# Optimization experiments

Hardware: AMD Instinct MI355X
Metric: run time of the kernel (lower is better)

Reference implementation:

```python
import jax, jax.numpy as jnp
import numpy as np

T, B, E = 2048, 2, 1024
H = 16
D = E // H


def setup_inputs() -> dict:
    key = jax.random.key(0)
    ks = jax.random.split(key, 7)
    s = 1.0 / np.sqrt(E)
    return {
        "query": jax.random.normal(ks[0], (T, B, E), jnp.float32),
        "key": jax.random.normal(ks[1], (T, B, E), jnp.float32),
        "value": jax.random.normal(ks[2], (T, B, E), jnp.float32),
        "in_proj_weight": jax.random.normal(ks[3], (3 * E, E), jnp.float32) * s,
        "in_proj_bias": jax.random.normal(ks[4], (3 * E,), jnp.float32) * 0.02,
        "out_proj_weight": jax.random.normal(ks[5], (E, E), jnp.float32) * s,
        "out_proj_bias": jax.random.normal(ks[6], (E,), jnp.float32) * 0.02,
    }


def reference(query, key, value, in_proj_weight, in_proj_bias, out_proj_weight, out_proj_bias):
    tgt_len, bsz, embed_dim = query.shape
    src_len = key.shape[0]
    head_dim = embed_dim // H
    # packed in-projection (F.linear: x @ W.T + b)
    w_q, w_k, w_v = jnp.split(in_proj_weight, 3, axis=0)
    b_q, b_k, b_v = jnp.split(in_proj_bias, 3, axis=0)
    q = query @ w_q.T + b_q   # [T, B, E]
    k = key @ w_k.T + b_k     # [S, B, E]
    v = value @ w_v.T + b_v   # [S, B, E]
    # [T,B,E] -> [B,H,T,D]
    q = q.reshape(tgt_len, bsz, H, head_dim).transpose(1, 2, 0, 3)
    k = k.reshape(src_len, bsz, H, head_dim).transpose(1, 2, 0, 3)
    v = v.reshape(src_len, bsz, H, head_dim).transpose(1, 2, 0, 3)
    scale = 1.0 / jnp.sqrt(jnp.asarray(head_dim, q.dtype))
    scores = jnp.einsum("bhtd,bhsd->bhts", q, k) * scale  # [B,H,T,S]
    attn_weights = jax.nn.softmax(scores, axis=-1)
    attn = jnp.einsum("bhts,bhsd->bhtd", attn_weights, v)  # [B,H,T,D]
    # [B,H,T,D] -> [T,B,E]
    attn = attn.transpose(2, 0, 1, 3).reshape(tgt_len, bsz, embed_dim)
    attn_output = attn @ out_proj_weight.T + out_proj_bias  # [T,B,E]
    # averaged attention weights over heads (average_attn_weights=True)
    avg_weights = jnp.sum(attn_weights, axis=1) / H  # [B,T,S]
    return attn_output, avg_weights
```

## Files before the change

### kernel.cpp

```cpp
#include <hip/hip_runtime.h>
#include <hip/hip_bf16.h>

typedef float  f32x2  __attribute__((ext_vector_type(2)));
typedef float  f32x4  __attribute__((ext_vector_type(4)));
typedef float  f32x16 __attribute__((ext_vector_type(16)));
typedef __bf16 bf16x8 __attribute__((ext_vector_type(8)));

#define MFMA16(A,B,C) __builtin_amdgcn_mfma_f32_16x16x32_bf16((A),(B),(C),0,0,0)
#define MFMA32(A,B,C) __builtin_amdgcn_mfma_f32_32x32x16_bf16((A),(B),(C),0,0,0)
#define EXP2(x) __builtin_amdgcn_exp2f(x)
#define LOG2(x) __builtin_amdgcn_logf(x)

static constexpr int Tn = 2048, Bn = 2, En = 1024, Hn = 16, Dn = 64;
static constexpr float kQScale = 0.125f * 1.4426950408889634f;

static __device__ __forceinline__ unsigned pack2(float a, float b) {
  union { __bf16 h[2]; unsigned u; } un;
  un.h[0] = (__bf16)a; un.h[1] = (__bf16)b;
  return un.u;
}

static __device__ __forceinline__ void gload_lds16(const void* g, void* l) {
  __builtin_amdgcn_global_load_lds(
      (const __attribute__((address_space(1))) void*)g,
      (__attribute__((address_space(3))) void*)l, 16, 0, 0);
}

__global__ __launch_bounds__(256)
void k_cvt(const float* __restrict__ q, const float* __restrict__ k,
           const float* __restrict__ v, const float* __restrict__ w3,
           const float* __restrict__ wo,
           __bf16* __restrict__ qb, __bf16* __restrict__ kb,
           __bf16* __restrict__ vb, __bf16* __restrict__ w3b,
           __bf16* __restrict__ wob)
{
  const size_t g = (size_t)blockIdx.x * 256 + threadIdx.x;
  const float* src;
  __bf16* dst;
  size_t off;
  if (g < 524288)        { src = q;  dst = qb;  off = g; }
  else if (g < 1048576)  { src = k;  dst = kb;  off = g - 524288; }
  else if (g < 1572864)  { src = v;  dst = vb;  off = g - 1048576; }
  else if (g < 1966080)  { src = w3; dst = w3b; off = g - 1572864; }
  else                   { src = wo; dst = wob; off = g - 1966080; }
  const float* p = src + off * 8;
  f32x4 a = *reinterpret_cast<const f32x4*>(p);
  f32x4 b = *reinterpret_cast<const f32x4*>(p + 4);
  bf16x8 o;
  #pragma unroll
  for (int e = 0; e < 4; ++e) { o[e] = (__bf16)a[e]; o[e + 4] = (__bf16)b[e]; }
  *reinterpret_cast<bf16x8*>(dst + off * 8) = o;
}

__global__ __launch_bounds__(256)
void k_qkv(const __bf16* __restrict__ Xq, const __bf16* __restrict__ Xk,
           const __bf16* __restrict__ Xv, const __bf16* __restrict__ W,
           const float* __restrict__ bias,
           __bf16* __restrict__ q_ws, __bf16* __restrict__ k_ws,
           __bf16* __restrict__ v_ws)
{
  __shared__ __align__(16) char a_lds[8192];
  __shared__ __align__(16) char b_lds[8192];
  const int tid = threadIdx.x;
  const int lane = tid & 63, w = tid >> 6;
  const int wr = w >> 1, wc = w & 1;
  const int ag = lane >> 4, lr = lane & 15;
  const int mBase = blockIdx.x * 128;
  const int oBase = blockIdx.y * 128;
  const int which = blockIdx.y >> 3;
  const __bf16* X  = (which == 0) ? Xq : ((which == 1) ? Xk : Xv);
  const __bf16* Wt = W + (size_t)oBase * En;
  __bf16* dst = (which == 0) ? q_ws : ((which == 1) ? k_ws : v_ws);
  const float oscale = (which == 0) ? kQScale : 1.0f;

  const int gA = w;
  char* laA0 = a_lds + gA * 2048;
  char* laA1 = a_lds + gA * 2048 + 1024;
  char* lbA0 = b_lds + gA * 2048;
  char* lbA1 = b_lds + gA * 2048 + 1024;
  const __bf16* pa0 = X  + (size_t)(mBase + lane) * En + gA * 8;
  const __bf16* pa1 = X  + (size_t)(mBase + 64 + lane) * En + gA * 8;
  const __bf16* pb0 = Wt + (size_t)(lane) * En + gA * 8;
  const __bf16* pb1 = Wt + (size_t)(64 + lane) * En + gA * 8;

  f32x4 acc[4][4];
  #pragma unroll
  for (int i = 0; i < 4; ++i)
    #pragma unroll
    for (int j = 0; j < 4; ++j) { f32x4 z = {0.f, 0.f, 0.f, 0.f}; acc[i][j] = z; }

  for (int kk = 0; kk < En; kk += 32) {
    __syncthreads();
    gload_lds16(pa0 + kk, laA0);
    gload_lds16(pa1 + kk, laA1);
    gload_lds16(pb0 + kk, lbA0);
    gload_lds16(pb1 + kk, lbA1);
    __syncthreads();
    bf16x8 af[4], bfr[4];
    #pragma unroll
    for (int mb = 0; mb < 4; ++mb)
      af[mb] = *(const bf16x8*)(a_lds + ag * 2048 + (wr * 64 + mb * 16 + lr) * 16);
    #pragma unroll
    for (int nb = 0; nb < 4; ++nb)
      bfr[nb] = *(const bf16x8*)(b_lds + ag * 2048 + (wc * 64 + nb * 16 + lr) * 16);
    #pragma unroll
    for (int mb = 0; mb < 4; ++mb)
      #pragma unroll
      for (int nb = 0; nb < 4; ++nb)
        acc[mb][nb] = MFMA16(af[mb], bfr[nb], acc[mb][nb]);
  }

  #pragma unroll
  for (int nb = 0; nb < 4; ++nb) {
    int oG = oBase + wc * 64 + nb * 16 + lr;
    float bv = bias[oG];
    int oS = oG & (En - 1);
    int h = oS >> 6, d = oS & 63;
    #pragma unroll
    for (int mb = 0; mb < 4; ++mb)
      #pragma unroll
      for (int r = 0; r < 4; ++r) {
        int i = mBase + wr * 64 + mb * 16 + ag * 4 + r;
        int t = i >> 1, b2 = i & 1;
        dst[(((size_t)(b2 * Hn + h)) * Tn + t) * Dn + d] =
            (__bf16)((acc[mb][nb][r] + bv) * oscale);
      }
  }
}

__global__ __launch_bounds__(256)
void k_transpose_v(const __bf16* __restrict__ v_ws, __bf16* __restrict__ vt_ws)
{
  __shared__ __bf16 tile[64][72];
  const int bh = blockIdx.x >> 5;
  const int tt = blockIdx.x & 31;
  const int tid = threadIdx.x;
  const __bf16* src = v_ws + ((size_t)bh * Tn + tt * 64) * Dn;
  #pragma unroll
  for (int it = 0; it < 2; ++it) {
    int gi = tid + it * 256;
    int row = gi >> 3, gg = gi & 7;
    *reinterpret_cast<bf16x8*>(&tile[row][gg * 8]) =
        *reinterpret_cast<const bf16x8*>(src + row * Dn + gg * 8);
  }
  __syncthreads();
  __bf16* dst = vt_ws + (size_t)bh * Dn * Tn + tt * 64;
  #pragma unroll
  for (int it = 0; it < 2; ++it) {
    int gi = tid + it * 256;
    int drow = gi >> 3, tg = gi & 7;
    bf16x8 vv;
    #pragma unroll
    for (int e = 0; e < 8; ++e) vv[e] = tile[tg * 8 + e][drow];
    *reinterpret_cast<bf16x8*>(dst + (size_t)drow * Tn + tg * 8) = vv;
  }
}

__global__ __launch_bounds__(256, 2)
void k_flash(const __bf16* __restrict__ q_ws, const __bf16* __restrict__ k_ws,
             const __bf16* __restrict__ vt_ws, __bf16* __restrict__ ctx,
             float* __restrict__ stats)
{
  __shared__ __align__(16) char kv_sm[2 * 16384];

  const int tid = threadIdx.x;
  const int lane = tid & 63, w = tid >> 6;
  const int tl = lane & 31, hi = lane >> 5;
  const int bh = blockIdx.x >> 4;
  const int qt = blockIdx.x & 15;
  const int t0w = qt * 128 + w * 32;

  const __bf16* kbase  = k_ws + (size_t)bh * Tn * Dn;
  const __bf16* vtbase = vt_ws + (size_t)bh * Dn * Tn;

  bf16x8 qf[4];
  {
    const __bf16* qrow = q_ws + ((size_t)bh * Tn + t0w + tl) * Dn + hi * 8;
    #pragma unroll
    for (int c = 0; c < 4; ++c)
      qf[c] = *reinterpret_cast<const bf16x8*>(qrow + c * 16);
  }

  f32x16 accO0, accO1;
  #pragma unroll
  for (int i = 0; i < 16; ++i) { accO0[i] = 0.f; accO1[i] = 0.f; }
  float m_run = -INFINITY, l_run = 0.f;

  const int r0 = tid >> 3, s0 = tid & 7;
  const int ldso = ((s0 ^ (r0 & 7)) << 4);
  const int ko0 = r0 * 128 + ldso;

  bf16x8 rk0 = *(const bf16x8*)(kbase + r0 * 64 + s0 * 8);
  bf16x8 rk1 = *(const bf16x8*)(kbase + (r0 + 32) * 64 + s0 * 8);
  bf16x8 rv0 = *(const bf16x8*)(vtbase + (size_t)r0 * Tn + s0 * 8);
  bf16x8 rv1 = *(const bf16x8*)(vtbase + (size_t)(r0 + 32) * Tn + s0 * 8);
  *(bf16x8*)(kv_sm + ko0) = rk0;
  *(bf16x8*)(kv_sm + ko0 + 4096) = rk1;
  *(bf16x8*)(kv_sm + 8192 + ko0) = rv0;
  *(bf16x8*)(kv_sm + 8192 + ko0 + 4096) = rv1;

  for (int st = 0; st < 32; ++st) {
    __syncthreads();
    const char* cur = kv_sm + (st & 1) * 16384;
    char* nxt = kv_sm + ((st + 1) & 1) * 16384;
    if (st + 1 < 32) {
      const __bf16* kn = kbase + (size_t)(st + 1) * 64 * Dn;
      const __bf16* vn = vtbase + (st + 1) * 64;
      rk0 = *(const bf16x8*)(kn + r0 * 64 + s0 * 8);
      rk1 = *(const bf16x8*)(kn + (r0 + 32) * 64 + s0 * 8);
      rv0 = *(const bf16x8*)(vn + (size_t)r0 * Tn + s0 * 8);
      rv1 = *(const bf16x8*)(vn + (size_t)(r0 + 32) * Tn + s0 * 8);
    }

    f32x16 sc0, sc1;
    #pragma unroll
    for (int i = 0; i < 16; ++i) { sc0[i] = 0.f; sc1[i] = 0.f; }
    const char* kr0 = cur + tl * 128;
    const char* kr1 = cur + (32 + tl) * 128;
    __builtin_amdgcn_s_setprio(1);
    #pragma unroll
    for (int c = 0; c < 4; ++c) {
      const int off = (((2 * c + hi) ^ (tl & 7)) << 4);
      sc0 = MFMA32(*(const bf16x8*)(kr0 + off), qf[c], sc0);
      sc1 = MFMA32(*(const bf16x8*)(kr1 + off), qf[c], sc1);
    }
    __builtin_amdgcn_s_setprio(0);

    float mx[8];
    #pragma unroll
    for (int i = 0; i < 8; ++i)
      mx[i] = fmaxf(fmaxf(sc0[i], sc0[i + 8]), fmaxf(sc1[i], sc1[i + 8]));
    float tm = fmaxf(fmaxf(fmaxf(mx[0], mx[1]), fmaxf(mx[2], mx[3])),
                     fmaxf(fmaxf(mx[4], mx[5]), fmaxf(mx[6], mx[7])));
    tm = fmaxf(tm, __shfl_xor(tm, 32, 64));
    if (__any(tm > m_run + 8.0f)) {
      const float mn = fmaxf(m_run, tm);
      const float es = EXP2(m_run - mn);
      m_run = mn;
      l_run *= es;
      #pragma unroll
      for (int q = 0; q < 4; ++q)
        #pragma unroll
        for (int rr = 0; rr < 4; ++rr) {
          const float e = __shfl(es, 8 * q + 4 * hi + rr, 32);
          accO0[q * 4 + rr] *= e;
          accO1[q * 4 + rr] *= e;
        }
    }
    #pragma unroll
    for (int i = 0; i < 16; ++i) {
      sc0[i] = EXP2(sc0[i] - m_run);
      sc1[i] = EXP2(sc1[i] - m_run);
    }
    float p0s = 0.f, p1s = 0.f, p2s = 0.f, p3s = 0.f;
    #pragma unroll
    for (int i = 0; i < 16; i += 4) {
      p0s += sc0[i]     + sc1[i];
      p1s += sc0[i + 1] + sc1[i + 1];
      p2s += sc0[i + 2] + sc1[i + 2];
      p3s += sc0[i + 3] + sc1[i + 3];
    }
    float rs = (p0s + p1s) + (p2s + p3s);
    rs += __shfl_xor(rs, 32, 64);
    l_run += rs;

    unsigned wA0[4], wB0[4], wA1[4], wB1[4];
    #pragma unroll
    for (int g = 0; g < 4; ++g) {
      wA0[g] = pack2(sc0[4 * g],     sc0[4 * g + 1]);
      wB0[g] = pack2(sc0[4 * g + 2], sc0[4 * g + 3]);
      wA1[g] = pack2(sc1[4 * g],     sc1[4 * g + 1]);
      wB1[g] = pack2(sc1[4 * g + 2], sc1[4 * g + 3]);
    }
    bf16x8 pa[2][2];
    #pragma unroll
    for (int sb = 0; sb < 2; ++sb) {
      const unsigned* WA = sb ? wA1 : wA0;
      const unsigned* WB = sb ? wB1 : wB0;
      #pragma unroll
      for (int c = 0; c < 2; ++c) {
        unsigned a0 = WA[2 * c], a1 = WA[2 * c + 1];
        unsigned b0 = WB[2 * c], b1 = WB[2 * c + 1];
        unsigned xa0 = __shfl_xor(a0, 32, 64);
        unsigned xa1 = __shfl_xor(a1, 32, 64);
        unsigned xb0 = __shfl_xor(b0, 32, 64);
        unsigned xb1 = __shfl_xor(b1, 32, 64);
        union { unsigned u[4]; bf16x8 v; } uu;
        uu.u[0] = hi ? xa1 : a0;
        uu.u[1] = hi ? xb1 : b0;
        uu.u[2] = hi ? a1 : xa0;
        uu.u[3] = hi ? b1 : xb0;
        pa[sb][c] = uu.v;
      }
    }

    const char* vr0 = cur + 8192 + tl * 128;
    const char* vr1 = cur + 8192 + (32 + tl) * 128;
    __builtin_amdgcn_s_setprio(1);
    #pragma unroll
    for (int sb = 0; sb < 2; ++sb)
      #pragma unroll
      for (int c = 0; c < 2; ++c) {
        const int off = (((sb * 4 + c * 2 + hi) ^ (tl & 7)) << 4);
        accO0 = MFMA32(pa[sb][c], *(const bf16x8*)(vr0 + off), accO0);
        accO1 = MFMA32(pa[sb][c], *(const bf16x8*)(vr1 + off), accO1);
      }
    __builtin_amdgcn_s_setprio(0);

    if (st + 1 < 32) {
      *(bf16x8*)(nxt + ko0) = rk0;
      *(bf16x8*)(nxt + ko0 + 4096) = rk1;
      *(bf16x8*)(nxt + 8192 + ko0) = rv0;
      *(bf16x8*)(nxt + 8192 + ko0 + 4096) = rv1;
    }
  }

  const float linv = 1.0f / l_run;
  const int b2 = bh >> 4, h = bh & 15;
  #pragma unroll
  for (int q = 0; q < 4; ++q)
    #pragma unroll
    for (int rr = 0; rr < 4; ++rr) {
      const float lv = __shfl(linv, 8 * q + 4 * hi + rr, 32);
      const int t = t0w + 8 * q + 4 * hi + rr;
      __bf16* cp = ctx + ((size_t)t * Bn + b2) * En + h * 64 + tl;
      cp[0]  = (__bf16)(accO0[q * 4 + rr] * lv);
      cp[32] = (__bf16)(accO1[q * 4 + rr] * lv);
    }
  if (hi == 0) {
    const int t = t0w + tl;
    f32x2 stv; stv[0] = m_run; stv[1] = l_run;
    *reinterpret_cast<f32x2*>(&stats[((size_t)bh * Tn + t) * 2]) = stv;
  }
}

__global__ __launch_bounds__(256)
void k_avgw(const __bf16* __restrict__ q_ws, const __bf16* __restrict__ k_ws,
            const float* __restrict__ stats, float* __restrict__ avg_out)
{
  __shared__ __align__(16) char q_sm[8192];
  __shared__ __align__(16) char k_sm[8192];
  __shared__ __align__(16) float adj_sm[16][64];

  const int tid = threadIdx.x;
  const int lane = tid & 63, w = tid >> 6;
  const int tl = lane & 31, hi = lane >> 5;
  const int b2 = blockIdx.x >> 10;
  const int tt = (blockIdx.x >> 5) & 31;
  const int ss = blockIdx.x & 31;
  const int thalf = (w >> 1) * 32, shalf = (w & 1) * 32;

  #pragma unroll
  for (int it = 0; it < 4; ++it) {
    int idx = tid + it * 256;
    int h = idx >> 6, trow = idx & 63;
    f32x2 sv = *(const f32x2*)&stats[(((size_t)(b2 * Hn + h)) * Tn + tt * 64 + trow) * 2];
    adj_sm[h][trow] = sv[0] + LOG2(16.0f * sv[1]);
  }

  const size_t hstride = (size_t)Tn * Dn;
  const __bf16* qb = q_ws + ((size_t)(b2 * Hn) * Tn + tt * 64) * Dn;
  const __bf16* kb = k_ws + ((size_t)(b2 * Hn) * Tn + ss * 64) * Dn;

  const int r0 = tid >> 3, s0 = tid & 7;
  const int ldso = ((s0 ^ (r0 & 7)) << 4);
  const int ko0 = r0 * 128 + ldso, ko1 = ko0 + 32 * 128;

  bf16x8 rq0 = *(const bf16x8*)(qb + r0 * 64 + s0 * 8);
  bf16x8 rq1 = *(const bf16x8*)(qb + (r0 + 32) * 64 + s0 * 8);
  bf16x8 rk0 = *(const bf16x8*)(kb + r0 * 64 + s0 * 8);
  bf16x8 rk1 = *(const bf16x8*)(kb + (r0 + 32) * 64 + s0 * 8);

  f32x16 avg;
  #pragma unroll
  for (int i = 0; i < 16; ++i) avg[i] = 0.f;

  const char* qr = q_sm + (thalf + tl) * 128;
  const char* kr = k_sm + (shalf + tl) * 128;

  for (int h = 0; h < Hn; ++h) {
    __syncthreads();
    *(bf16x8*)(q_sm + ko0) = rq0;
    *(bf16x8*)(q_sm + ko1) = rq1;
    *(bf16x8*)(k_sm + ko0) = rk0;
    *(bf16x8*)(k_sm + ko1) = rk1;
    __syncthreads();
    if (h + 1 < Hn) {
      const __bf16* qn = qb + (size_t)(h + 1) * hstride;
      const __bf16* kn = kb + (size_t)(h + 1) * hstride;
      rq0 = *(const bf16x8*)(qn + r0 * 64 + s0 * 8);
      rq1 = *(const bf16x8*)(qn + (r0 + 32) * 64 + s0 * 8);
      rk0 = *(const bf16x8*)(kn + r0 * 64 + s0 * 8);
      rk1 = *(const bf16x8*)(kn + (r0 + 32) * 64 + s0 * 8);
    }

    f32x16 sc;
    #pragma unroll
    for (int i = 0; i < 16; ++i) sc[i] = 0.f;
    #pragma unroll
    for (int c = 0; c < 4; ++c) {
      const int off = (((2 * c + hi) ^ (tl & 7)) << 4);
      sc = MFMA32(*(const bf16x8*)(qr + off), *(const bf16x8*)(kr + off), sc);
    }

    #pragma unroll
    for (int q = 0; q < 4; ++q) {
      f32x4 ad = *(const f32x4*)&adj_sm[h][thalf + 8 * q + 4 * hi];
      #pragma unroll
      for (int r = 0; r < 4; ++r)
        avg[q * 4 + r] += EXP2(sc[q * 4 + r] - ad[r]);
    }
  }

  #pragma unroll
  for (int q = 0; q < 4; ++q)
    #pragma unroll
    for (int r = 0; r < 4; ++r) {
      int t = tt * 64 + thalf + 8 * q + 4 * hi + r;
      int s = ss * 64 + shalf + tl;
      avg_out[((size_t)(b2 * Tn + t)) * Tn + s] = avg[q * 4 + r];
    }
}

__global__ __launch_bounds__(256)
void k_outproj(const __bf16* __restrict__ ctx, const __bf16* __restrict__ W,
               const float* __restrict__ bias, float* __restrict__ out)
{
  __shared__ __align__(16) char a_lds[8192];
  __shared__ __align__(16) char b_lds[8192];
  const int tid = threadIdx.x;
  const int lane = tid & 63, w = tid >> 6;
  const int wr = w >> 1, wc = w & 1;
  const int ag = lane >> 4, lr = lane & 15;
  const int mBase = blockIdx.x * 128;
  const int oBase = blockIdx.y * 128;
  const __bf16* Wt = W + (size_t)oBase * En;

  const int gA = w;
  char* laA0 = a_lds + gA * 2048;
  char* laA1 = a_lds + gA * 2048 + 1024;
  char* lbA0 = b_lds + gA * 2048;
  char* lbA1 = b_lds + gA * 2048 + 1024;
  const __bf16* pa0 = ctx + (size_t)(mBase + lane) * En + gA * 8;
  const __bf16* pa1 = ctx + (size_t)(mBase + 64 + lane) * En + gA * 8;
  const __bf16* pb0 = Wt + (size_t)(lane) * En + gA * 8;
  const __bf16* pb1 = Wt + (size_t)(64 + lane) * En + gA * 8;

  f32x4 acc[4][4];
  #pragma unroll
  for (int i = 0; i < 4; ++i)
    #pragma unroll
    for (int j = 0; j < 4; ++j) { f32x4 z = {0.f,0.f,0.f,0.f}; acc[i][j] = z; }

  for (int kk = 0; kk < En; kk += 32) {
    __syncthreads();
    gload_lds16(pa0 + kk, laA0);
    gload_lds16(pa1 + kk, laA1);
    gload_lds16(pb0 + kk, lbA0);
    gload_lds16(pb1 + kk, lbA1);
    __syncthreads();
    bf16x8 af[4], bfr[4];
    #pragma unroll
    for (int mb = 0; mb < 4; ++mb)
      af[mb] = *(const bf16x8*)(a_lds + ag * 2048 + (wr * 64 + mb * 16 + lr) * 16);
    #pragma unroll
    for (int nb = 0; nb < 4; ++nb)
      bfr[nb] = *(const bf16x8*)(b_lds + ag * 2048 + (wc * 64 + nb * 16 + lr) * 16);
    #pragma unroll
    for (int mb = 0; mb < 4; ++mb)
      #pragma unroll
      for (int nb = 0; nb < 4; ++nb)
        acc[mb][nb] = MFMA16(af[mb], bfr[nb], acc[mb][nb]);
  }

  #pragma unroll
  for (int nb = 0; nb < 4; ++nb) {
    int o = oBase + wc * 64 + nb * 16 + lr;
    float bv = bias[o];
    #pragma unroll
    for (int mb = 0; mb < 4; ++mb)
      #pragma unroll
      for (int r = 0; r < 4; ++r) {
        int i = mBase + wr * 64 + mb * 16 + ag * 4 + r;
        out[(size_t)i * En + o] = acc[mb][nb][r] + bv;
      }
  }
}

extern "C" void kernel_launch(void* const* d_in, const int* in_sizes, int n_in,
                              void* d_out, int out_size, void* d_ws, size_t ws_size,
                              hipStream_t stream)
{
  (void)in_sizes; (void)n_in; (void)out_size; (void)ws_size;
  const float* query = (const float*)d_in[0];
  const float* key   = (const float*)d_in[1];
  const float* value = (const float*)d_in[2];
  const float* in_w  = (const float*)d_in[3];
  const float* in_b  = (const float*)d_in[4];
  const float* out_w = (const float*)d_in[5];
  const float* out_b = (const float*)d_in[6];

  float* attn_out = (float*)d_out;
  float* avg_out  = (float*)d_out + (size_t)Tn * Bn * En;

  char* ws = (char*)d_ws;
  const size_t MB = 1u << 20;
  __bf16* q_ws  = (__bf16*)(ws);
  __bf16* k_ws  = (__bf16*)(ws + 8 * MB);
  __bf16* v_ws  = (__bf16*)(ws + 16 * MB);
  __bf16* vt_ws = (__bf16*)(ws + 24 * MB);
  __bf16* ctx   = (__bf16*)(ws + 32 * MB);
  float*  stats = (float*)(ws + 40 * MB);
  __bf16* xq_bf = vt_ws;
  __bf16* xk_bf = ctx;
  __bf16* xv_bf = (__bf16*)(ws + 40 * MB + 512 * 1024);
  __bf16* w3_bf = (__bf16*)(ws + 48 * MB + 512 * 1024);
  __bf16* wo_bf = (__bf16*)(ws + 54 * MB + 512 * 1024);

  k_cvt<<<8192, 256, 0, stream>>>(query, key, value, in_w, out_w,
                                  xq_bf, xk_bf, xv_bf, w3_bf, wo_bf);
  k_qkv<<<dim3(32, 24), 256, 0, stream>>>(xq_bf, xk_bf, xv_bf, w3_bf, in_b,
                                          q_ws, k_ws, v_ws);
  k_transpose_v<<<1024, 256, 0, stream>>>(v_ws, vt_ws);
  k_flash<<<512, 256, 0, stream>>>(q_ws, k_ws, vt_ws, ctx, stats);
  k_avgw<<<2048, 256, 0, stream>>>(q_ws, k_ws, stats, avg_out);
  k_outproj<<<dim3(32, 8), 256, 0, stream>>>(ctx, wo_bf, out_b, attn_out);
}
```

Before: 212.5 us.

## Double-buffer GEMM/avgw LDS, compute softmax rowsum via MFMA, use permlane32 swap

The QKV and output-projection GEMMs get double-buffered LDS with prefetch of the next K tile, which removes one barrier per step. The attention-weight kernel likewise double-buffers its Q/K tiles across heads. In the flash kernel the row sum is now accumulated by an extra MFMA against a ones vector instead of a VALU reduction plus shuffle. The P-fragment repack uses v_permlane32_swap instead of four cross-lane shuffles, and the flash kernel precomputes the per-row log-sum adjustment so avgw reads one float. This adds LDS usage and extra MFMA work per iteration in exchange for fewer VALU ops and barriers.

```diff
diff --git a/kernel.cpp b/kernel.cpp
--- a/kernel.cpp
+++ b/kernel.cpp
@@ -59,8 +59,8 @@
            __bf16* __restrict__ q_ws, __bf16* __restrict__ k_ws,
            __bf16* __restrict__ v_ws)
 {
-  __shared__ __align__(16) char a_lds[8192];
-  __shared__ __align__(16) char b_lds[8192];
+  __shared__ __align__(16) char a_lds[2][8192];
+  __shared__ __align__(16) char b_lds[2][8192];
   const int tid = threadIdx.x;
   const int lane = tid & 63, w = tid >> 6;
   const int wr = w >> 1, wc = w & 1;
@@ -74,10 +74,6 @@
   const float oscale = (which == 0) ? kQScale : 1.0f;
 
   const int gA = w;
-  char* laA0 = a_lds + gA * 2048;
-  char* laA1 = a_lds + gA * 2048 + 1024;
-  char* lbA0 = b_lds + gA * 2048;
-  char* lbA1 = b_lds + gA * 2048 + 1024;
   const __bf16* pa0 = X  + (size_t)(mBase + lane) * En + gA * 8;
   const __bf16* pa1 = X  + (size_t)(mBase + 64 + lane) * En + gA * 8;
   const __bf16* pb0 = Wt + (size_t)(lane) * En + gA * 8;
@@ -89,25 +85,34 @@
     #pragma unroll
     for (int j = 0; j < 4; ++j) { f32x4 z = {0.f, 0.f, 0.f, 0.f}; acc[i][j] = z; }
 
-  for (int kk = 0; kk < En; kk += 32) {
-    __syncthreads();
-    gload_lds16(pa0 + kk, laA0);
-    gload_lds16(pa1 + kk, laA1);
-    gload_lds16(pb0 + kk, lbA0);
-    gload_lds16(pb1 + kk, lbA1);
-    __syncthreads();
+  gload_lds16(pa0, &a_lds[0][gA * 2048]);
+  gload_lds16(pa1, &a_lds[0][gA * 2048 + 1024]);
+  gload_lds16(pb0, &b_lds[0][gA * 2048]);
+  gload_lds16(pb1, &b_lds[0][gA * 2048 + 1024]);
+  __syncthreads();
+
+  for (int kt = 0; kt < 32; ++kt) {
+    const int cur = kt & 1, nxt = cur ^ 1;
+    if (kt + 1 < 32) {
+      const int kk = (kt + 1) * 32;
+      gload_lds16(pa0 + kk, &a_lds[nxt][gA * 2048]);
+      gload_lds16(pa1 + kk, &a_lds[nxt][gA * 2048 + 1024]);
+      gload_lds16(pb0 + kk, &b_lds[nxt][gA * 2048]);
+      gload_lds16(pb1 + kk, &b_lds[nxt][gA * 2048 + 1024]);
+    }
     bf16x8 af[4], bfr[4];
     #pragma unroll
     for (int mb = 0; mb < 4; ++mb)
-      af[mb] = *(const bf16x8*)(a_lds + ag * 2048 + (wr * 64 + mb * 16 + lr) * 16);
+      af[mb] = *(const bf16x8*)(&a_lds[cur][ag * 2048 + (wr * 64 + mb * 16 + lr) * 16]);
     #pragma unroll
     for (int nb = 0; nb < 4; ++nb)
-      bfr[nb] = *(const bf16x8*)(b_lds + ag * 2048 + (wc * 64 + nb * 16 + lr) * 16);
+      bfr[nb] = *(const bf16x8*)(&b_lds[cur][ag * 2048 + (wc * 64 + nb * 16 + lr) * 16]);
     #pragma unroll
     for (int mb = 0; mb < 4; ++mb)
       #pragma unroll
       for (int nb = 0; nb < 4; ++nb)
         acc[mb][nb] = MFMA16(af[mb], bfr[nb], acc[mb][nb]);
+    __syncthreads();
   }
 
   #pragma unroll
@@ -159,7 +164,7 @@
 __global__ __launch_bounds__(256, 2)
 void k_flash(const __bf16* __restrict__ q_ws, const __bf16* __restrict__ k_ws,
              const __bf16* __restrict__ vt_ws, __bf16* __restrict__ ctx,
-             float* __restrict__ stats)
+             float* __restrict__ adj_g)
 {
   __shared__ __align__(16) char kv_sm[2 * 16384];
 
@@ -181,10 +186,15 @@
       qf[c] = *reinterpret_cast<const bf16x8*>(qrow + c * 16);
   }
 
-  f32x16 accO0, accO1;
-  #pragma unroll
-  for (int i = 0; i < 16; ++i) { accO0[i] = 0.f; accO1[i] = 0.f; }
-  float m_run = -INFINITY, l_run = 0.f;
+  union { unsigned u[4]; bf16x8 v; } onu;
+  #pragma unroll
+  for (int j = 0; j < 4; ++j) onu.u[j] = 0x3F803F80u;
+  const bf16x8 kOne = onu.v;
+
+  f32x16 accO0, accO1, accL;
+  #pragma unroll
+  for (int i = 0; i < 16; ++i) { accO0[i] = 0.f; accO1[i] = 0.f; accL[i] = 0.f; }
+  float m_run = -INFINITY;
 
   const int r0 = tid >> 3, s0 = tid & 7;
   const int ldso = ((s0 ^ (r0 & 7)) << 4);
@@ -237,7 +247,6 @@
       const float mn = fmaxf(m_run, tm);
       const float es = EXP2(m_run - mn);
       m_run = mn;
-      l_run *= es;
       #pragma unroll
       for (int q = 0; q < 4; ++q)
         #pragma unroll
@@ -245,6 +254,7 @@
           const float e = __shfl(es, 8 * q + 4 * hi + rr, 32);
           accO0[q * 4 + rr] *= e;
           accO1[q * 4 + rr] *= e;
+          accL[q * 4 + rr] *= e;
         }
     }
     #pragma unroll
@@ -252,17 +262,6 @@
       sc0[i] = EXP2(sc0[i] - m_run);
       sc1[i] = EXP2(sc1[i] - m_run);
     }
-    float p0s = 0.f, p1s = 0.f, p2s = 0.f, p3s = 0.f;
-    #pragma unroll
-    for (int i = 0; i < 16; i += 4) {
-      p0s += sc0[i]     + sc1[i];
-      p1s += sc0[i + 1] + sc1[i + 1];
-      p2s += sc0[i + 2] + sc1[i + 2];
-      p3s += sc0[i + 3] + sc1[i + 3];
-    }
-    float rs = (p0s + p1s) + (p2s + p3s);
-    rs += __shfl_xor(rs, 32, 64);
-    l_run += rs;
 
     unsigned wA0[4], wB0[4], wA1[4], wB1[4];
     #pragma unroll
@@ -279,17 +278,12 @@
       const unsigned* WB = sb ? wB1 : wB0;
       #pragma unroll
       for (int c = 0; c < 2; ++c) {
-        unsigned a0 = WA[2 * c], a1 = WA[2 * c + 1];
-        unsigned b0 = WB[2 * c], b1 = WB[2 * c + 1];
-        unsigned xa0 = __shfl_xor(a0, 32, 64);
-        unsigned xa1 = __shfl_xor(a1, 32, 64);
-        unsigned xb0 = __shfl_xor(b0, 32, 64);
-        unsigned xb1 = __shfl_xor(b1, 32, 64);
+        unsigned w0 = WA[2 * c], w2 = WA[2 * c + 1];
+        unsigned w1 = WB[2 * c], w3 = WB[2 * c + 1];
+        asm("v_permlane32_swap_b32 %0, %1" : "+v"(w0), "+v"(w2));
+        asm("v_permlane32_swap_b32 %0, %1" : "+v"(w1), "+v"(w3));
         union { unsigned u[4]; bf16x8 v; } uu;
-        uu.u[0] = hi ? xa1 : a0;
-        uu.u[1] = hi ? xb1 : b0;
-        uu.u[2] = hi ? a1 : xa0;
-        uu.u[3] = hi ? b1 : xb0;
+        uu.u[0] = w0; uu.u[1] = w1; uu.u[2] = w2; uu.u[3] = w3;
         pa[sb][c] = uu.v;
       }
     }
@@ -304,6 +298,7 @@
         const int off = (((sb * 4 + c * 2 + hi) ^ (tl & 7)) << 4);
         accO0 = MFMA32(pa[sb][c], *(const bf16x8*)(vr0 + off), accO0);
         accO1 = MFMA32(pa[sb][c], *(const bf16x8*)(vr1 + off), accO1);
+        accL  = MFMA32(pa[sb][c], kOne, accL);
       }
     __builtin_amdgcn_s_setprio(0);
 
@@ -315,31 +310,38 @@
     }
   }
 
-  const float linv = 1.0f / l_run;
   const int b2 = bh >> 4, h = bh & 15;
+  float adjv[16];
   #pragma unroll
   for (int q = 0; q < 4; ++q)
     #pragma unroll
     for (int rr = 0; rr < 4; ++rr) {
-      const float lv = __shfl(linv, 8 * q + 4 * hi + rr, 32);
+      const int j = q * 4 + rr;
+      const float lv = 1.0f / accL[j];
       const int t = t0w + 8 * q + 4 * hi + rr;
       __bf16* cp = ctx + ((size_t)t * Bn + b2) * En + h * 64 + tl;
-      cp[0]  = (__bf16)(accO0[q * 4 + rr] * lv);
-      cp[32] = (__bf16)(accO1[q * 4 + rr] * lv);
-    }
-  if (hi == 0) {
-    const int t = t0w + tl;
-    f32x2 stv; stv[0] = m_run; stv[1] = l_run;
-    *reinterpret_cast<f32x2*>(&stats[((size_t)bh * Tn + t) * 2]) = stv;
+      cp[0]  = (__bf16)(accO0[j] * lv);
+      cp[32] = (__bf16)(accO1[j] * lv);
+      const float mrow = __shfl(m_run, 8 * q + 4 * hi + rr, 32);
+      adjv[j] = mrow + LOG2(16.0f * accL[j]);
+    }
+  if (tl == 0) {
+    #pragma unroll
+    for (int q = 0; q < 4; ++q)
+      #pragma unroll
+      for (int rr = 0; rr < 4; ++rr) {
+        const int t = t0w + 8 * q + 4 * hi + rr;
+        adj_g[(size_t)bh * Tn + t] = adjv[q * 4 + rr];
+      }
   }
 }
 
 __global__ __launch_bounds__(256)
 void k_avgw(const __bf16* __restrict__ q_ws, const __bf16* __restrict__ k_ws,
-            const float* __restrict__ stats, float* __restrict__ avg_out)
-{
-  __shared__ __align__(16) char q_sm[8192];
-  __shared__ __align__(16) char k_sm[8192];
+            const float* __restrict__ adj_g, float* __restrict__ avg_out)
+{
+  __shared__ __align__(16) char q_sm[2][8192];
+  __shared__ __align__(16) char k_sm[2][8192];
   __shared__ __align__(16) float adj_sm[16][64];
 
   const int tid = threadIdx.x;
@@ -354,8 +356,7 @@
   for (int it = 0; it < 4; ++it) {
     int idx = tid + it * 256;
     int h = idx >> 6, trow = idx & 63;
-    f32x2 sv = *(const f32x2*)&stats[(((size_t)(b2 * Hn + h)) * Tn + tt * 64 + trow) * 2];
-    adj_sm[h][trow] = sv[0] + LOG2(16.0f * sv[1]);
+    adj_sm[h][trow] = adj_g[((size_t)(b2 * Hn + h)) * Tn + tt * 64 + trow];
   }
 
   const size_t hstride = (size_t)Tn * Dn;
@@ -364,39 +365,41 @@
 
   const int r0 = tid >> 3, s0 = tid & 7;
   const int ldso = ((s0 ^ (r0 & 7)) << 4);
-  const int ko0 = r0 * 128 + ldso, ko1 = ko0 + 32 * 128;
+  const int ko0 = r0 * 128 + ldso;
 
   bf16x8 rq0 = *(const bf16x8*)(qb + r0 * 64 + s0 * 8);
   bf16x8 rq1 = *(const bf16x8*)(qb + (r0 + 32) * 64 + s0 * 8);
   bf16x8 rk0 = *(const bf16x8*)(kb + r0 * 64 + s0 * 8);
   bf16x8 rk1 = *(const bf16x8*)(kb + (r0 + 32) * 64 + s0 * 8);
+  *(bf16x8*)(q_sm[0] + ko0) = rq0;
+  *(bf16x8*)(q_sm[0] + ko0 + 4096) = rq1;
+  *(bf16x8*)(k_sm[0] + ko0) = rk0;
+  *(bf16x8*)(k_sm[0] + ko0 + 4096) = rk1;
 
   f32x16 avg;
   #pragma unroll
   for (int i = 0; i < 16; ++i) avg[i] = 0.f;
-
-  const char* qr = q_sm + (thalf + tl) * 128;
-  const char* kr = k_sm + (shalf + tl) * 128;
 
   for (int h = 0; h < Hn; ++h) {
     __syncthreads();
-    *(bf16x8*)(q_sm + ko0) = rq0;
-    *(bf16x8*)(q_sm + ko1) = rq1;
-    *(bf16x8*)(k_sm + ko0) = rk0;
-    *(bf16x8*)(k_sm + ko1) = rk1;
-    __syncthreads();
+    const char* qc = q_sm[h & 1];
+    const char* kc = k_sm[h & 1];
+    char* qn = q_sm[(h + 1) & 1];
+    char* kn = k_sm[(h + 1) & 1];
     if (h + 1 < Hn) {
-      const __bf16* qn = qb + (size_t)(h + 1) * hstride;
-      const __bf16* kn = kb + (size_t)(h + 1) * hstride;
-      rq0 = *(const bf16x8*)(qn + r0 * 64 + s0 * 8);
-      rq1 = *(const bf16x8*)(qn + (r0 + 32) * 64 + s0 * 8);
-      rk0 = *(const bf16x8*)(kn + r0 * 64 + s0 * 8);
-      rk1 = *(const bf16x8*)(kn + (r0 + 32) * 64 + s0 * 8);
+      const __bf16* qp = qb + (size_t)(h + 1) * hstride;
+      const __bf16* kp = kb + (size_t)(h + 1) * hstride;
+      rq0 = *(const bf16x8*)(qp + r0 * 64 + s0 * 8);
+      rq1 = *(const bf16x8*)(qp + (r0 + 32) * 64 + s0 * 8);
+      rk0 = *(const bf16x8*)(kp + r0 * 64 + s0 * 8);
+      rk1 = *(const bf16x8*)(kp + (r0 + 32) * 64 + s0 * 8);
     }
 
     f32x16 sc;
     #pragma unroll
     for (int i = 0; i < 16; ++i) sc[i] = 0.f;
+    const char* qr = qc + (thalf + tl) * 128;
+    const char* kr = kc + (shalf + tl) * 128;
     #pragma unroll
     for (int c = 0; c < 4; ++c) {
       const int off = (((2 * c + hi) ^ (tl & 7)) << 4);
@@ -409,6 +412,13 @@
       #pragma unroll
       for (int r = 0; r < 4; ++r)
         avg[q * 4 + r] += EXP2(sc[q * 4 + r] - ad[r]);
+    }
+
+    if (h + 1 < Hn) {
+      *(bf16x8*)(qn + ko0) = rq0;
+      *(bf16x8*)(qn + ko0 + 4096) = rq1;
+      *(bf16x8*)(kn + ko0) = rk0;
+      *(bf16x8*)(kn + ko0 + 4096) = rk1;
     }
   }
 
@@ -426,8 +436,8 @@
 void k_outproj(const __bf16* __restrict__ ctx, const __bf16* __restrict__ W,
                const float* __restrict__ bias, float* __restrict__ out)
 {
-  __shared__ __align__(16) char a_lds[8192];
-  __shared__ __align__(16) char b_lds[8192];
+  __shared__ __align__(16) char a_lds[2][8192];
+  __shared__ __align__(16) char b_lds[2][8192];
   const int tid = threadIdx.x;
   const int lane = tid & 63, w = tid >> 6;
   const int wr = w >> 1, wc = w & 1;
@@ -437,10 +447,6 @@
   const __bf16* Wt = W + (size_t)oBase * En;
 
   const int gA = w;
-  char* laA0 = a_lds + gA * 2048;
-  char* laA1 = a_lds + gA * 2048 + 1024;
-  char* lbA0 = b_lds + gA * 2048;
-  char* lbA1 = b_lds + gA * 2048 + 1024;
   const __bf16* pa0 = ctx + (size_t)(mBase + lane) * En + gA * 8;
   const __bf16* pa1 = ctx + (size_t)(mBase + 64 + lane) * En + gA * 8;
   const __bf16* pb0 = Wt + (size_t)(lane) * En + gA * 8;
@@ -452,25 +458,34 @@
     #pragma unroll
     for (int j = 0; j < 4; ++j) { f32x4 z = {0.f,0.f,0.f,0.f}; acc[i][j] = z; }
 
-  for (int kk = 0; kk < En; kk += 32) {
-    __syncthreads();
-    gload_lds16(pa0 + kk, laA0);
-    gload_lds16(pa1 + kk, laA1);
-    gload_lds16(pb0 + kk, lbA0);
-    gload_lds16(pb1 + kk, lbA1);
-    __syncthreads();
+  gload_lds16(pa0, &a_lds[0][gA * 2048]);
+  gload_lds16(pa1, &a_lds[0][gA * 2048 + 1024]);
+  gload_lds16(pb0, &b_lds[0][gA * 2048]);
+  gload_lds16(pb1, &b_lds[0][gA * 2048 + 1024]);
+  __syncthreads();
+
+  for (int kt = 0; kt < 32; ++kt) {
+    const int cur = kt & 1, nxt = cur ^ 1;
+    if (kt + 1 < 32) {
+      const int kk = (kt + 1) * 32;
+      gload_lds16(pa0 + kk, &a_lds[nxt][gA * 2048]);
+      gload_lds16(pa1 + kk, &a_lds[nxt][gA * 2048 + 1024]);
+      gload_lds16(pb0 + kk, &b_lds[nxt][gA * 2048]);
+      gload_lds16(pb1 + kk, &b_lds[nxt][gA * 2048 + 1024]);
+    }
     bf16x8 af[4], bfr[4];
     #pragma unroll
     for (int mb = 0; mb < 4; ++mb)
-      af[mb] = *(const bf16x8*)(a_lds + ag * 2048 + (wr * 64 + mb * 16 + lr) * 16);
+      af[mb] = *(const bf16x8*)(&a_lds[cur][ag * 2048 + (wr * 64 + mb * 16 + lr) * 16]);
     #pragma unroll
     for (int nb = 0; nb < 4; ++nb)
-      bfr[nb] = *(const bf16x8*)(b_lds + ag * 2048 + (wc * 64 + nb * 16 + lr) * 16);
+      bfr[nb] = *(const bf16x8*)(&b_lds[cur][ag * 2048 + (wc * 64 + nb * 16 + lr) * 16]);
     #pragma unroll
     for (int mb = 0; mb < 4; ++mb)
       #pragma unroll
       for (int nb = 0; nb < 4; ++nb)
         acc[mb][nb] = MFMA16(af[mb], bfr[nb], acc[mb][nb]);
+    __syncthreads();
   }
 
   #pragma unroll
@@ -510,7 +525,7 @@
   __bf16* v_ws  = (__bf16*)(ws + 16 * MB);
   __bf16* vt_ws = (__bf16*)(ws + 24 * MB);
   __bf16* ctx   = (__bf16*)(ws + 32 * MB);
-  float*  stats = (float*)(ws + 40 * MB);
+  float*  adj_g = (float*)(ws + 40 * MB);
   __bf16* xq_bf = vt_ws;
   __bf16* xk_bf = ctx;
   __bf16* xv_bf = (__bf16*)(ws + 40 * MB + 512 * 1024);
@@ -522,7 +537,7 @@
   k_qkv<<<dim3(32, 24), 256, 0, stream>>>(xq_bf, xk_bf, xv_bf, w3_bf, in_b,
                                           q_ws, k_ws, v_ws);
   k_transpose_v<<<1024, 256, 0, stream>>>(v_ws, vt_ws);
-  k_flash<<<512, 256, 0, stream>>>(q_ws, k_ws, vt_ws, ctx, stats);
-  k_avgw<<<2048, 256, 0, stream>>>(q_ws, k_ws, stats, avg_out);
+  k_flash<<<512, 256, 0, stream>>>(q_ws, k_ws, vt_ws, ctx, adj_g);
+  k_avgw<<<2048, 256, 0, stream>>>(q_ws, k_ws, adj_g, avg_out);
   k_outproj<<<dim3(32, 8), 256, 0, stream>>>(ctx, wo_bf, out_b, attn_out);
 }
```

Measured after the change: 201.2 us. 5.3% less time.
